# Performance work log

Hardware: AMD Instinct MI355X
Metric: run time of the kernel (lower is better)

The kernel has to match this reference:

```python
import jax, jax.numpy as jnp
import numpy as np

N, E, F0, H = 100000, 3200000, 256, 128
TEMP = 2.0
ALPHA = 0.2  # leaky relu slope
EPS_BN = 1e-5
EPS_LN = 1e-5


def spmm(vals, row, col, X):
    # sparse [N,N] @ dense [N,D] via gather + segment_sum
    return jax.ops.segment_sum(vals[:, None] * X[col], row, num_segments=N)


def batchnorm(h, g, b):
    mu = jnp.mean(h, axis=0, keepdims=True)
    var = jnp.var(h, axis=0, keepdims=True)
    return (h - mu) * jax.lax.rsqrt(var + EPS_BN) * g + b


def layernorm(h, g, b):
    mu = jnp.mean(h, axis=-1, keepdims=True)
    var = jnp.var(h, axis=-1, keepdims=True)
    return (h - mu) * jax.lax.rsqrt(var + EPS_LN) * g + b


def setup_inputs() -> dict:
    key = jax.random.key(0)
    ks = jax.random.split(key, 32)
    x = jax.random.normal(ks[0], (N, F0), dtype=jnp.float32)
    edge_row = jax.random.randint(ks[1], (E,), 0, N)
    edge_col = jax.random.randint(ks[2], (E,), 0, N)
    adj_vals = jax.random.uniform(ks[3], (E,), dtype=jnp.float32) / 32.0  # ~normalized adj
    sf = lambda k, sh: jax.random.normal(k, sh, dtype=jnp.float32) * 0.05
    in_dim = 3 * F0 + 1
    return {
        "x": x, "edge_row": edge_row, "edge_col": edge_col, "adj_vals": adj_vals,
        # LowPassExtractor (GCN)
        "W_gc1": sf(ks[4], (F0, 2 * H)), "b_gc1": jnp.zeros((2 * H,), jnp.float32),
        "bn1_g": jnp.ones((2 * H,), jnp.float32), "bn1_b": jnp.zeros((2 * H,), jnp.float32),
        "W_gc2": sf(ks[5], (2 * H, H)), "b_gc2": jnp.zeros((H,), jnp.float32),
        "bn2_g": jnp.ones((H,), jnp.float32), "bn2_b": jnp.zeros((H,), jnp.float32),
        # Gating
        "Wg1": sf(ks[6], (in_dim, H)), "bg1": jnp.zeros((H,), jnp.float32),
        "ln_g": jnp.ones((H,), jnp.float32), "ln_b": jnp.zeros((H,), jnp.float32),
        "Wg2": sf(ks[7], (H, 2)), "bg2": jnp.zeros((2,), jnp.float32),
        # HighPassExpert
        "Wxp": sf(ks[8], (F0, H)), "bxp": jnp.zeros((H,), jnp.float32),
        "res_scale": jnp.asarray(1.0, jnp.float32),
        "rn_g": jnp.ones((H,), jnp.float32), "rn_b": jnp.zeros((H,), jnp.float32),
        "Wq": sf(ks[9], (H, H)), "Wk": sf(ks[10], (H, H)), "Wv": sf(ks[11], (H, H)),
    }


def reference(x, edge_row, edge_col, adj_vals,
              W_gc1, b_gc1, bn1_g, bn1_b, W_gc2, b_gc2, bn2_g, bn2_b,
              Wg1, bg1, ln_g, ln_b, Wg2, bg2,
              Wxp, bxp, res_scale, rn_g, rn_b, Wq, Wk, Wv):
    # ---- LowPassExtractor: two GCN layers (spmm(adj, xW)+b) with batchnorm+relu
    h1 = jax.nn.relu(batchnorm(spmm(adj_vals, edge_row, edge_col, x @ W_gc1) + b_gc1, bn1_g, bn1_b))
    low = jax.nn.relu(batchnorm(spmm(adj_vals, edge_row, edge_col, h1 @ W_gc2) + b_gc2, bn2_g, bn2_b))

    # ---- Gating: neighborhood stats via spmm
    AX = spmm(adj_vals, edge_row, edge_col, x)
    deg = jax.ops.segment_sum(adj_vals, edge_row, num_segments=N)[:, None]
    x_mean = AX / (deg + 1e-8)
    AX2 = spmm(adj_vals, edge_row, edge_col, x * x)
    var = AX2 / (deg + 1e-8) - x_mean * x_mean
    x_std = jnp.sqrt(jnp.clip(var, 0.0))
    x_cat = jnp.concatenate([x, AX - x, x_std, deg], axis=1)  # [N, 3*F0+1]
    hg = jax.nn.relu(layernorm(x_cat @ Wg1 + bg1, ln_g, ln_b))
    gate = jax.nn.softmax((hg @ Wg2 + bg2) / TEMP, axis=1)  # [N, 2]

    # ---- HighPassExpert: GAT-style sparse attention on normalized residual
    residual = layernorm(res_scale * (x @ Wxp + bxp - low), rn_g, rn_b)
    Q, K, V = residual @ Wq, residual @ Wk, residual @ Wv
    scores = jnp.sum(Q[edge_row] * K[edge_col], axis=1) / jnp.sqrt(jnp.float32(H))
    exp_s = jnp.exp(jnp.where(scores > 0, scores, ALPHA * scores))
    denom = jax.ops.segment_sum(exp_s, edge_row, num_segments=N)
    attn = exp_s / (denom[edge_row] + 1e-16)
    high = jax.ops.segment_sum(attn[:, None] * V[edge_col], edge_row, num_segments=N)

    output = gate[:, 0:1] * low + gate[:, 1:2] * high
    return output, gate, low, high
```

## Files before the change

### kernel.cpp

```cpp
#include <hip/hip_runtime.h>

#define F0 256
#define HD 128
#define NP 100352

typedef unsigned short u16;
typedef __attribute__((ext_vector_type(8))) short short8;
typedef __attribute__((ext_vector_type(4))) float f32x4;

__device__ inline float bf2f(u16 u) {
    union { unsigned int i; float f; } v; v.i = ((unsigned int)u) << 16; return v.f;
}
__device__ inline u16 f2bf(float f) {
    union { float f; unsigned int i; } v; v.f = f;
    unsigned int r = v.i + 0x7FFF + ((v.i >> 16) & 1);
    return (u16)(r >> 16);
}

__device__ inline float rsum16(float v) {
    v += __shfl_xor(v, 1); v += __shfl_xor(v, 2);
    v += __shfl_xor(v, 4); v += __shfl_xor(v, 8);
    return v;
}

#define GLOAD16(gp, lp) __builtin_amdgcn_global_load_lds( \
    (const __attribute__((address_space(1))) void*)(gp), \
    (__attribute__((address_space(3))) void*)(lp), 16, 0, 0)

__global__ void k_hist_rank(const int* __restrict__ row, int* __restrict__ counts,
                            int* __restrict__ rank, int E) {
    int e = blockIdx.x * blockDim.x + threadIdx.x;
    if (e < E) rank[e] = atomicAdd(&counts[row[e]], 1);
}

__global__ void k_scan_blk(const int* __restrict__ counts, int* __restrict__ scan_out,
                           int* __restrict__ partials, int n) {
    __shared__ int wsum[16];
    int t = threadIdx.x;
    int i = blockIdx.x * 1024 + t;
    int v = (i < n) ? counts[i] : 0;
    int lane = t & 63, w = t >> 6;
    #pragma unroll
    for (int off = 1; off < 64; off <<= 1) { int u = __shfl_up(v, off); if (lane >= off) v += u; }
    if (lane == 63) wsum[w] = v;
    __syncthreads();
    if (t < 16) {
        int s = wsum[t];
        #pragma unroll
        for (int off = 1; off < 16; off <<= 1) { int u = __shfl_up(s, off); if (t >= off) s += u; }
        wsum[t] = s;
    }
    __syncthreads();
    int add = (w > 0) ? wsum[w - 1] : 0;
    if (i < n) scan_out[i] = v + add;
    if (t == 1023) partials[blockIdx.x] = wsum[15];
}

__global__ void k_scan_part(int* partials, int nb) {
    __shared__ int ws2[2];
    int t = threadIdx.x;
    int v = (t < nb) ? partials[t] : 0;
    int lane = t & 63, w = t >> 6;
    #pragma unroll
    for (int off = 1; off < 64; off <<= 1) { int u = __shfl_up(v, off); if (lane >= off) v += u; }
    if (lane == 63) ws2[w] = v;
    __syncthreads();
    if (w == 1) v += ws2[0];
    if (t < nb) partials[t] = v;
}

__global__ void k_scan_add(int* __restrict__ row_ptr, const int* __restrict__ partials, int n) {
    int b = blockIdx.x;
    int i = b * 1024 + threadIdx.x;
    if (b == 0 && threadIdx.x == 0) row_ptr[0] = 0;
    int add = (b > 0) ? partials[b - 1] : 0;
    if (i < n) row_ptr[1 + i] += add;
}

__global__ void k_scatter_direct(const int* __restrict__ row, const int* __restrict__ ecol,
                                 const float* __restrict__ avals, const int* __restrict__ rank,
                                 const int* __restrict__ row_ptr, int2* __restrict__ cv, int E) {
    int e = blockIdx.x * blockDim.x + threadIdx.x;
    if (e >= E) return;
    int r = row[e];
    int c = __builtin_nontemporal_load(ecol + e);
    float v = __builtin_nontemporal_load(avals + e);
    int rk = __builtin_nontemporal_load(rank + e);
    int pos = row_ptr[r] + rk;
    cv[pos] = make_int2(c, __float_as_int(v));
}

__global__ void k_cast_x(const float* __restrict__ x, u16* __restrict__ xb, int total4) {
    int i = blockIdx.x * blockDim.x + threadIdx.x;
    if (i >= total4) return;
    float4 v = ((const float4*)x)[i];
    ((ushort4*)xb)[i] = make_ushort4(f2bf(v.x), f2bf(v.y), f2bf(v.z), f2bf(v.w));
}

__global__ void k_prep_w(const float* __restrict__ W_gc1, const float* __restrict__ W_gc2,
                         const float* __restrict__ Wg1, const float* __restrict__ Wxp,
                         const float* __restrict__ Wq, const float* __restrict__ Wk,
                         const float* __restrict__ Wv,
                         u16* Wgc1t, u16* Wgc2t, u16* Wdt, u16* W1t, u16* W2t,
                         u16* Wxpt, u16* Wqt, u16* Wkt, u16* Wvt) {
    int z = blockIdx.z;
    int idx = blockIdx.x * 256 + threadIdx.x;
    if (z == 0) { if (idx < 65536) { int n = idx >> 8, k = idx & 255; Wgc1t[idx] = f2bf(W_gc1[k * 256 + n]); } }
    else if (z == 1) { if (idx < 32768) { int n = idx >> 8, k = idx & 255; Wgc2t[idx] = f2bf(W_gc2[k * 128 + n]); } }
    else if (z == 2) { if (idx < 32768) { int n = idx >> 8, k = idx & 255; Wdt[idx] = f2bf(Wg1[k * 128 + n] - Wg1[(k + 256) * 128 + n]); } }
    else if (z == 3) { if (idx < 32768) { int n = idx >> 8, k = idx & 255; W1t[idx] = f2bf(Wg1[(k + 256) * 128 + n]); } }
    else if (z == 4) { if (idx < 32768) { int n = idx >> 8, k = idx & 255; W2t[idx] = f2bf(Wg1[(k + 512) * 128 + n]); } }
    else if (z == 5) { if (idx < 32768) { int n = idx >> 8, k = idx & 255; Wxpt[idx] = f2bf(Wxp[k * 128 + n]); } }
    else if (z == 6) { if (idx < 16384) { int n = idx >> 7, k = idx & 127; Wqt[idx] = f2bf(Wq[k * 128 + n]); } }
    else if (z == 7) { if (idx < 16384) { int n = idx >> 7, k = idx & 127; Wkt[idx] = f2bf(Wk[k * 128 + n]); } }
    else if (z == 8) { if (idx < 16384) { int n = idx >> 7, k = idx & 127; Wvt[idx] = f2bf(Wv[k * 128 + n]); } }
}

__global__ void k_spmm_x2(const u16* __restrict__ Xb, const int* __restrict__ row_ptr,
                          const int2* __restrict__ cv,
                          u16* __restrict__ AXb, u16* __restrict__ XSTDb,
                          float* __restrict__ deg, int N) {
    int wid = blockIdx.x * 4 + (threadIdx.x >> 6);
    if (wid >= N) return;
    int lane = threadIdx.x & 63;
    float a0 = 0, a1 = 0, a2 = 0, a3 = 0;
    float q0 = 0, q1 = 0, q2 = 0, q3 = 0, d = 0;
    int s = row_ptr[wid], e = row_ptr[wid + 1];
    int j = s;
    for (; j + 7 < e; j += 8) {
        int2 cc[8]; ushort4 xb[8];
        #pragma unroll
        for (int t = 0; t < 8; ++t) cc[t] = cv[j + t];
        #pragma unroll
        for (int t = 0; t < 8; ++t) xb[t] = *(const ushort4*)(Xb + (size_t)cc[t].x * F0 + lane * 4);
        #pragma unroll
        for (int t = 0; t < 8; ++t) {
            float x0 = bf2f(xb[t].x), x1 = bf2f(xb[t].y), x2 = bf2f(xb[t].z), x3 = bf2f(xb[t].w);
            float vv = __int_as_float(cc[t].y);
            a0 += vv * x0; a1 += vv * x1; a2 += vv * x2; a3 += vv * x3;
            q0 += vv * x0 * x0; q1 += vv * x1 * x1; q2 += vv * x2 * x2; q3 += vv * x3 * x3;
            d += vv;
        }
    }
    for (; j < e; ++j) {
        int2 cc = cv[j];
        float v0 = __int_as_float(cc.y);
        ushort4 xb0 = *(const ushort4*)(Xb + (size_t)cc.x * F0 + lane * 4);
        float x0 = bf2f(xb0.x), x1 = bf2f(xb0.y), x2 = bf2f(xb0.z), x3 = bf2f(xb0.w);
        a0 += v0 * x0; a1 += v0 * x1; a2 += v0 * x2; a3 += v0 * x3;
        q0 += v0 * x0 * x0; q1 += v0 * x1 * x1; q2 += v0 * x2 * x2; q3 += v0 * x3 * x3;
        d += v0;
    }
    float inv = 1.0f / (d + 1e-8f);
    float m0 = a0 * inv, m1 = a1 * inv, m2 = a2 * inv, m3 = a3 * inv;
    float s0 = sqrtf(fmaxf(q0 * inv - m0 * m0, 0.f));
    float s1 = sqrtf(fmaxf(q1 * inv - m1 * m1, 0.f));
    float s2 = sqrtf(fmaxf(q2 * inv - m2 * m2, 0.f));
    float s3 = sqrtf(fmaxf(q3 * inv - m3 * m3, 0.f));
    *(ushort4*)(AXb + (size_t)wid * F0 + lane * 4) = make_ushort4(f2bf(a0), f2bf(a1), f2bf(a2), f2bf(a3));
    *(ushort4*)(XSTDb + (size_t)wid * F0 + lane * 4) = make_ushort4(f2bf(s0), f2bf(s1), f2bf(s2), f2bf(s3));
    if (lane == 0) deg[wid] = d;
}

__global__ void k_spmm128(const u16* __restrict__ Xb, const int* __restrict__ row_ptr,
                          const int2* __restrict__ cv, u16* __restrict__ OUT, int N) {
    int wid = blockIdx.x * 4 + (threadIdx.x >> 6);
    if (wid >= N) return;
    int lane = threadIdx.x & 63;
    float a0 = 0, a1 = 0;
    int s = row_ptr[wid], e = row_ptr[wid + 1];
    int j = s;
    for (; j + 7 < e; j += 8) {
        int2 cc[8]; ushort2 xb[8];
        #pragma unroll
        for (int t = 0; t < 8; ++t) cc[t] = cv[j + t];
        #pragma unroll
        for (int t = 0; t < 8; ++t) xb[t] = *(const ushort2*)(Xb + (size_t)cc[t].x * HD + lane * 2);
        #pragma unroll
        for (int t = 0; t < 8; ++t) {
            float vv = __int_as_float(cc[t].y);
            a0 += vv * bf2f(xb[t].x); a1 += vv * bf2f(xb[t].y);
        }
    }
    for (; j < e; ++j) {
        int2 cc = cv[j];
        float v0 = __int_as_float(cc.y);
        ushort2 x0 = *(const ushort2*)(Xb + (size_t)cc.x * HD + lane * 2);
        a0 += v0 * bf2f(x0.x); a1 += v0 * bf2f(x0.y);
    }
    *(ushort2*)(OUT + (size_t)wid * HD + lane * 2) = make_ushort2(f2bf(a0), f2bf(a1));
}

__device__ inline void mm_core(const u16* __restrict__ A, const u16* __restrict__ Bt,
                               int K, int ldA, int ldB, int m0, int n0,
                               u16* As, u16* Bs, f32x4 acc[4][4]) {
    int t = threadIdx.x, w = t >> 6, l = t & 63;
    int wr = (w >> 1) * 64, wc = (w & 1) * 64;
    int aoff = (wr + (l & 15)) * 32 + (l >> 4) * 8;
    int boff = (wc + (l & 15)) * 32 + (l >> 4) * 8;
    for (int k0 = 0; k0 < K; k0 += 32) {
        __syncthreads();
        #pragma unroll
        for (int s = 0; s < 2; ++s) {
            int i = s * 256 + t;
            int row = i >> 2, ch = i & 3;
            GLOAD16(A + (size_t)(m0 + row) * ldA + k0 + ch * 8, As + i * 8);
            GLOAD16(Bt + (size_t)(n0 + row) * ldB + k0 + ch * 8, Bs + i * 8);
        }
        __syncthreads();
        short8 af[4], bfr[4];
        #pragma unroll
        for (int i = 0; i < 4; ++i) af[i] = *(const short8*)(As + aoff + i * 16 * 32);
        #pragma unroll
        for (int j = 0; j < 4; ++j) bfr[j] = *(const short8*)(Bs + boff + j * 16 * 32);
        #pragma unroll
        for (int i = 0; i < 4; ++i)
            #pragma unroll
            for (int j = 0; j < 4; ++j)
                acc[i][j] = __builtin_amdgcn_mfma_f32_16x16x32_bf16(af[i], bfr[j], acc[i][j], 0, 0, 0);
    }
}

__device__ inline void mm_zero(f32x4 acc[4][4]) {
    #pragma unroll
    for (int i = 0; i < 4; ++i)
        #pragma unroll
        for (int j = 0; j < 4; ++j)
            acc[i][j] = (f32x4){0.f, 0.f, 0.f, 0.f};
}

__global__ __launch_bounds__(256) void k_mm_bf(const u16* __restrict__ A, const u16* __restrict__ Bt,
                                               u16* __restrict__ C, int M, int K, int Nc) {
    __shared__ __align__(16) u16 As[128 * 32];
    __shared__ __align__(16) u16 Bs[128 * 32];
    int m0 = blockIdx.x * 128, n0 = blockIdx.y * 128;
    f32x4 acc[4][4]; mm_zero(acc);
    mm_core(A, Bt, K, K, K, m0, n0, As, Bs, acc);
    int t = threadIdx.x, w = t >> 6, l = t & 63;
    int rbase = m0 + (w >> 1) * 64 + (l >> 4) * 4;
    int cbase = n0 + (w & 1) * 64 + (l & 15);
    #pragma unroll
    for (int j = 0; j < 4; ++j)
        #pragma unroll
        for (int i = 0; i < 4; ++i)
            #pragma unroll
            for (int r = 0; r < 4; ++r) {
                int row = rbase + i * 16 + r;
                if (row < M) C[(size_t)row * Nc + cbase + j * 16] = f2bf(acc[i][j][r]);
            }
}

__global__ __launch_bounds__(256) void k_mm_gate(const u16* A0, const u16* A1, const u16* A2,
                                                 const u16* B0, const u16* B1, const u16* B2,
                                                 const float* __restrict__ bg1,
                                                 const float* __restrict__ wlast,
                                                 const float* __restrict__ deg,
                                                 const float* __restrict__ ln_g,
                                                 const float* __restrict__ ln_b,
                                                 const float* __restrict__ Wg2,
                                                 const float* __restrict__ bg2,
                                                 float* __restrict__ gate, int M) {
    __shared__ __align__(16) u16 As[128 * 32];
    __shared__ __align__(16) u16 Bs[128 * 32];
    __shared__ float ps1[2][128], ps2[2][128], pt0[2][128], pt1[2][128];
    int m0 = blockIdx.x * 128;
    f32x4 acc[4][4]; mm_zero(acc);
    mm_core(A0, B0, 256, 256, 256, m0, 0, As, Bs, acc);
    mm_core(A1, B1, 256, 256, 256, m0, 0, As, Bs, acc);
    mm_core(A2, B2, 256, 256, 256, m0, 0, As, Bs, acc);
    int t = threadIdx.x, w = t >> 6, l = t & 63;
    int hcol = w & 1;
    int lr0 = (w >> 1) * 64 + (l >> 4) * 4;
    int cbase = hcol * 64 + (l & 15);
    float wl[4], bg[4], lg[4], lb[4], wa[4], wb_[4];
    #pragma unroll
    for (int j = 0; j < 4; ++j) {
        int col = cbase + j * 16;
        wl[j] = wlast[col]; bg[j] = bg1[col];
        lg[j] = ln_g[col];  lb[j] = ln_b[col];
        wa[j] = Wg2[col * 2 + 0]; wb_[j] = Wg2[col * 2 + 1];
    }
    #pragma unroll
    for (int i = 0; i < 4; ++i)
        #pragma unroll
        for (int r = 0; r < 4; ++r) {
            int row = m0 + lr0 + i * 16 + r;
            float dgv = (row < M) ? deg[row] : 0.f;
            float s1 = 0.f, s2 = 0.f;
            #pragma unroll
            for (int j = 0; j < 4; ++j) {
                float h = acc[i][j][r] + bg[j] + dgv * wl[j];
                acc[i][j][r] = h;
                s1 += h; s2 += h * h;
            }
            s1 = rsum16(s1); s2 = rsum16(s2);
            if ((l & 15) == 0) { ps1[hcol][lr0 + i * 16 + r] = s1; ps2[hcol][lr0 + i * 16 + r] = s2; }
        }
    __syncthreads();
    #pragma unroll
    for (int i = 0; i < 4; ++i)
        #pragma unroll
        for (int r = 0; r < 4; ++r) {
            int lr = lr0 + i * 16 + r;
            float s1 = ps1[0][lr] + ps1[1][lr];
            float s2 = ps2[0][lr] + ps2[1][lr];
            float mu = s1 * (1.f / 128.f);
            float var = s2 * (1.f / 128.f) - mu * mu;
            float is = 1.0f / sqrtf(var + 1e-5f);
            float t0 = 0.f, t1 = 0.f;
            #pragma unroll
            for (int j = 0; j < 4; ++j) {
                float y = fmaxf((acc[i][j][r] - mu) * is * lg[j] + lb[j], 0.f);
                t0 += y * wa[j]; t1 += y * wb_[j];
            }
            t0 = rsum16(t0); t1 = rsum16(t1);
            if ((l & 15) == 0) { pt0[hcol][lr] = t0; pt1[hcol][lr] = t1; }
        }
    __syncthreads();
    if (hcol == 0 && (l & 15) == 0) {
        float b20 = bg2[0], b21 = bg2[1];
        #pragma unroll
        for (int i = 0; i < 4; ++i)
            #pragma unroll
            for (int r = 0; r < 4; ++r) {
                int lr = lr0 + i * 16 + r;
                int row = m0 + lr;
                if (row >= M) continue;
                float t0 = (pt0[0][lr] + pt0[1][lr] + b20) * 0.5f;
                float t1 = (pt1[0][lr] + pt1[1][lr] + b21) * 0.5f;
                float m = fmaxf(t0, t1);
                float e0 = __expf(t0 - m), e1 = __expf(t1 - m);
                float inv = 1.0f / (e0 + e1);
                gate[(size_t)row * 2 + 0] = e0 * inv;
                gate[(size_t)row * 2 + 1] = e1 * inv;
            }
    }
}

__global__ __launch_bounds__(256) void k_mm_xp(const u16* __restrict__ A, const u16* __restrict__ Bt,
                                               const float* __restrict__ bias,
                                               const float* __restrict__ low,
                                               const float* __restrict__ g,
                                               const float* __restrict__ b,
                                               const float* __restrict__ rs_ptr,
                                               u16* __restrict__ resid, int M) {
    __shared__ __align__(16) u16 As[128 * 32];
    __shared__ __align__(16) u16 Bs[128 * 32];
    __shared__ float ps1[2][128], ps2[2][128];
    int m0 = blockIdx.x * 128;
    f32x4 acc[4][4]; mm_zero(acc);
    mm_core(A, Bt, 256, 256, 256, m0, 0, As, Bs, acc);
    int t = threadIdx.x, w = t >> 6, l = t & 63;
    int hcol = w & 1;
    int lr0 = (w >> 1) * 64 + (l >> 4) * 4;
    int cbase = hcol * 64 + (l & 15);
    float rs = rs_ptr[0];
    float bx[4], lg[4], lb[4];
    #pragma unroll
    for (int j = 0; j < 4; ++j) {
        int col = cbase + j * 16;
        bx[j] = bias[col]; lg[j] = g[col]; lb[j] = b[col];
    }
    #pragma unroll
    for (int i = 0; i < 4; ++i)
        #pragma unroll
        for (int r = 0; r < 4; ++r) {
            int row = m0 + lr0 + i * 16 + r;
            float s1 = 0.f, s2 = 0.f;
            #pragma unroll
            for (int j = 0; j < 4; ++j) {
                float lv = (row < M) ? low[(size_t)row * 128 + cbase + j * 16] : 0.f;
                float h = rs * (acc[i][j][r] + bx[j] - lv);
                acc[i][j][r] = h;
                s1 += h; s2 += h * h;
            }
            s1 = rsum16(s1); s2 = rsum16(s2);
            if ((l & 15) == 0) { ps1[hcol][lr0 + i * 16 + r] = s1; ps2[hcol][lr0 + i * 16 + r] = s2; }
        }
    __syncthreads();
    #pragma unroll
    for (int i = 0; i < 4; ++i)
        #pragma unroll
        for (int r = 0; r < 4; ++r) {
            int lr = lr0 + i * 16 + r;
            int row = m0 + lr;
            float s1 = ps1[0][lr] + ps1[1][lr];
            float s2 = ps2[0][lr] + ps2[1][lr];
            float mu = s1 * (1.f / 128.f);
            float var = s2 * (1.f / 128.f) - mu * mu;
            float is = 1.0f / sqrtf(var + 1e-5f);
            if (row < M) {
                #pragma unroll
                for (int j = 0; j < 4; ++j) {
                    float y = (acc[i][j][r] - mu) * is * lg[j] + lb[j];
                    resid[(size_t)row * 128 + cbase + j * 16] = f2bf(y);
                }
            }
        }
}

__global__ __launch_bounds__(256) void k_mm_qkv3(const u16* __restrict__ A,
                                                 const u16* __restrict__ Wqt,
                                                 const u16* __restrict__ Wkt,
                                                 const u16* __restrict__ Wvt,
                                                 u16* __restrict__ Qb, u16* __restrict__ KV, int M) {
    __shared__ __align__(16) u16 As[4][128 * 32];
    __shared__ __align__(16) u16 Bs[128 * 32];
    int m0 = blockIdx.x * 128;
    int t = threadIdx.x, w = t >> 6, l = t & 63;
    #pragma unroll
    for (int c = 0; c < 4; ++c)
        #pragma unroll
        for (int s = 0; s < 2; ++s) {
            int i = s * 256 + t;
            int row = i >> 2, ch = i & 3;
            GLOAD16(A + (size_t)(m0 + row) * 128 + c * 32 + ch * 8, As[c] + i * 8);
        }
    int wr = (w >> 1) * 64, wc = (w & 1) * 64;
    int aoff = (wr + (l & 15)) * 32 + (l >> 4) * 8;
    int boff = (wc + (l & 15)) * 32 + (l >> 4) * 8;
    int rbase = m0 + (w >> 1) * 64 + (l >> 4) * 4;
    int cbase = (w & 1) * 64 + (l & 15);
    #pragma unroll
    for (int z = 0; z < 3; ++z) {
        const u16* Bt = (z == 0) ? Wqt : (z == 1) ? Wkt : Wvt;
        f32x4 acc[4][4]; mm_zero(acc);
        for (int k0 = 0; k0 < 128; k0 += 32) {
            __syncthreads();
            #pragma unroll
            for (int s = 0; s < 2; ++s) {
                int i = s * 256 + t;
                int row = i >> 2, ch = i & 3;
                GLOAD16(Bt + (size_t)row * 128 + k0 + ch * 8, Bs + i * 8);
            }
            __syncthreads();
            const u16* Ac = As[k0 >> 5];
            short8 af[4], bfr[4];
            #pragma unroll
            for (int i = 0; i < 4; ++i) af[i] = *(const short8*)(Ac + aoff + i * 16 * 32);
            #pragma unroll
            for (int j = 0; j < 4; ++j) bfr[j] = *(const short8*)(Bs + boff + j * 16 * 32);
            #pragma unroll
            for (int i = 0; i < 4; ++i)
                #pragma unroll
                for (int j = 0; j < 4; ++j)
                    acc[i][j] = __builtin_amdgcn_mfma_f32_16x16x32_bf16(af[i], bfr[j], acc[i][j], 0, 0, 0);
        }
        if (z == 0) {
            #pragma unroll
            for (int j = 0; j < 4; ++j)
                #pragma unroll
                for (int i = 0; i < 4; ++i)
                    #pragma unroll
                    for (int r = 0; r < 4; ++r) {
                        int row = rbase + i * 16 + r;
                        if (row < M) Qb[(size_t)row * 128 + cbase + j * 16] = f2bf(acc[i][j][r]);
                    }
        } else {
            int coff = (z == 1) ? 0 : 128;
            #pragma unroll
            for (int j = 0; j < 4; ++j)
                #pragma unroll
                for (int i = 0; i < 4; ++i)
                    #pragma unroll
                    for (int r = 0; r < 4; ++r) {
                        int row = rbase + i * 16 + r;
                        if (row < M) KV[(size_t)row * 256 + coff + cbase + j * 16] = f2bf(acc[i][j][r]);
                    }
        }
    }
}

__global__ void k_bn_stats_bf(const u16* __restrict__ H, double* __restrict__ stats, int N, int C) {
    int t = threadIdx.x;
    int rpt = 256 / C;
    int rsub = t / C;
    int col = t - rsub * C;
    double s = 0.0, q = 0.0;
    for (long r = (long)blockIdx.x * rpt + rsub; r < N; r += (long)gridDim.x * rpt) {
        float v = bf2f(H[(size_t)r * C + col]);
        s += v; q += (double)v * v;
    }
    __shared__ double sh_s[256], sh_q[256];
    sh_s[t] = s; sh_q[t] = q;
    __syncthreads();
    if (t < C) {
        for (int k = 1; k < rpt; ++k) { s += sh_s[t + k * C]; q += sh_q[t + k * C]; }
        atomicAdd(&stats[t], s);
        atomicAdd(&stats[C + t], q);
    }
}

__global__ void k_bn_fin(const double* __restrict__ stats, const float* __restrict__ g,
                         const float* __restrict__ b, float* __restrict__ scale,
                         float* __restrict__ shift, int C, double invN) {
    int t = threadIdx.x;
    if (t >= C) return;
    double mean = stats[t] * invN;
    double var = stats[C + t] * invN - mean * mean;
    float sc = (float)((double)g[t] / sqrt(var + 1e-5));
    scale[t] = sc;
    shift[t] = b[t] - (float)mean * sc;
}

__global__ void k_bn_relu_bb(const u16* __restrict__ in, u16* __restrict__ out,
                             const float* __restrict__ scale, const float* __restrict__ shift,
                             int total4, int cmask4) {
    int i = blockIdx.x * blockDim.x + threadIdx.x;
    if (i >= total4) return;
    int c4 = i & cmask4;
    ushort4 v = ((const ushort4*)in)[i];
    float4 sc = ((const float4*)scale)[c4];
    float4 sh = ((const float4*)shift)[c4];
    ((ushort4*)out)[i] = make_ushort4(
        f2bf(fmaxf(bf2f(v.x) * sc.x + sh.x, 0.f)), f2bf(fmaxf(bf2f(v.y) * sc.y + sh.y, 0.f)),
        f2bf(fmaxf(bf2f(v.z) * sc.z + sh.z, 0.f)), f2bf(fmaxf(bf2f(v.w) * sc.w + sh.w, 0.f)));
}

__global__ void k_bn_relu_bf(const u16* __restrict__ in, float* __restrict__ out,
                             const float* __restrict__ scale, const float* __restrict__ shift,
                             int total4, int cmask4) {
    int i = blockIdx.x * blockDim.x + threadIdx.x;
    if (i >= total4) return;
    int c4 = i & cmask4;
    ushort4 v = ((const ushort4*)in)[i];
    float4 sc = ((const float4*)scale)[c4];
    float4 sh = ((const float4*)shift)[c4];
    ((float4*)out)[i] = make_float4(
        fmaxf(bf2f(v.x) * sc.x + sh.x, 0.f), fmaxf(bf2f(v.y) * sc.y + sh.y, 0.f),
        fmaxf(bf2f(v.z) * sc.z + sh.z, 0.f), fmaxf(bf2f(v.w) * sc.w + sh.w, 0.f));
}

__global__ void k_attn_aggr(const u16* __restrict__ Qb, const u16* __restrict__ KV,
                            const int* __restrict__ row_ptr, const int2* __restrict__ cv,
                            const float* __restrict__ gate, const float* __restrict__ low,
                            float* __restrict__ high, float* __restrict__ outp, int N) {
    int wid = blockIdx.x * 4 + (threadIdx.x >> 6);
    if (wid >= N) return;
    int lane = threadIdx.x & 63;
    int sub = lane & 15;
    int g = lane >> 4;
    float qs[8];
    {
        short8 q8 = *(const short8*)(Qb + (size_t)wid * HD + sub * 8);
        #pragma unroll
        for (int k = 0; k < 8; ++k) qs[k] = bf2f((u16)q8[k]);
    }
    float2 qv;
    {
        ushort2 qt = *(const ushort2*)(Qb + (size_t)wid * HD + lane * 2);
        qv.x = bf2f(qt.x); qv.y = bf2f(qt.y);
    }
    float n0 = 0, n1 = 0, den = 0;
    int s = row_ptr[wid], e = row_ptr[wid + 1];
    int j = s;
    for (; j + 7 < e; j += 8) {
        int cg0 = cv[j + g].x;
        int cg1 = cv[j + 4 + g].x;
        short8 ka = *(const short8*)(KV + (size_t)cg0 * 256 + sub * 8);
        short8 kb = *(const short8*)(KV + (size_t)cg1 * 256 + sub * 8);
        float p0 = qs[0] * bf2f((u16)ka[0]) + qs[1] * bf2f((u16)ka[1])
                 + qs[2] * bf2f((u16)ka[2]) + qs[3] * bf2f((u16)ka[3])
                 + qs[4] * bf2f((u16)ka[4]) + qs[5] * bf2f((u16)ka[5])
                 + qs[6] * bf2f((u16)ka[6]) + qs[7] * bf2f((u16)ka[7]);
        float p1 = qs[0] * bf2f((u16)kb[0]) + qs[1] * bf2f((u16)kb[1])
                 + qs[2] * bf2f((u16)kb[2]) + qs[3] * bf2f((u16)kb[3])
                 + qs[4] * bf2f((u16)kb[4]) + qs[5] * bf2f((u16)kb[5])
                 + qs[6] * bf2f((u16)kb[6]) + qs[7] * bf2f((u16)kb[7]);
        p0 += __shfl_xor(p0, 1); p1 += __shfl_xor(p1, 1);
        p0 += __shfl_xor(p0, 2); p1 += __shfl_xor(p1, 2);
        p0 += __shfl_xor(p0, 4); p1 += __shfl_xor(p1, 4);
        p0 += __shfl_xor(p0, 8); p1 += __shfl_xor(p1, 8);
        float sc0 = p0 * 0.08838834764831845f;
        float sc1 = p1 * 0.08838834764831845f;
        float ls0 = sc0 > 0.f ? sc0 : 0.2f * sc0;
        float ls1 = sc1 > 0.f ? sc1 : 0.2f * sc1;
        float ex0 = __expf(ls0);
        float ex1 = __expf(ls1);
        float exb[8]; int cb[8];
        #pragma unroll
        for (int t = 0; t < 4; ++t) {
            exb[t]     = __shfl(ex0, t << 4); cb[t]     = __shfl(cg0, t << 4);
            exb[4 + t] = __shfl(ex1, t << 4); cb[4 + t] = __shfl(cg1, t << 4);
        }
        ushort2 vb[8];
        #pragma unroll
        for (int t = 0; t < 8; ++t) vb[t] = *(const ushort2*)(KV + (size_t)cb[t] * 256 + 128 + lane * 2);
        #pragma unroll
        for (int t = 0; t < 8; ++t) {
            n0 += exb[t] * bf2f(vb[t].x);
            n1 += exb[t] * bf2f(vb[t].y);
            den += exb[t];
        }
    }
    for (; j + 3 < e; j += 4) {
        int cg = cv[j + g].x;
        short8 kk = *(const short8*)(KV + (size_t)cg * 256 + sub * 8);
        float p = qs[0] * bf2f((u16)kk[0]) + qs[1] * bf2f((u16)kk[1])
                + qs[2] * bf2f((u16)kk[2]) + qs[3] * bf2f((u16)kk[3])
                + qs[4] * bf2f((u16)kk[4]) + qs[5] * bf2f((u16)kk[5])
                + qs[6] * bf2f((u16)kk[6]) + qs[7] * bf2f((u16)kk[7]);
        p += __shfl_xor(p, 1); p += __shfl_xor(p, 2);
        p += __shfl_xor(p, 4); p += __shfl_xor(p, 8);
        float sc = p * 0.08838834764831845f;
        float ls = sc > 0.f ? sc : 0.2f * sc;
        float ex = __expf(ls);
        float exb[4]; int cb[4];
        #pragma unroll
        for (int t = 0; t < 4; ++t) { exb[t] = __shfl(ex, t << 4); cb[t] = __shfl(cg, t << 4); }
        ushort2 vb[4];
        #pragma unroll
        for (int t = 0; t < 4; ++t) vb[t] = *(const ushort2*)(KV + (size_t)cb[t] * 256 + 128 + lane * 2);
        #pragma unroll
        for (int t = 0; t < 4; ++t) {
            n0 += exb[t] * bf2f(vb[t].x);
            n1 += exb[t] * bf2f(vb[t].y);
            den += exb[t];
        }
    }
    for (; j < e; ++j) {
        int c0 = cv[j].x;
        ushort2 kb0 = *(const ushort2*)(KV + (size_t)c0 * 256 + lane * 2);
        ushort2 vb0 = *(const ushort2*)(KV + (size_t)c0 * 256 + 128 + lane * 2);
        float sc0 = qv.x * bf2f(kb0.x) + qv.y * bf2f(kb0.y);
        #pragma unroll
        for (int off = 32; off > 0; off >>= 1) sc0 += __shfl_xor(sc0, off);
        float p = sc0 * 0.08838834764831845f;
        float ls = p > 0.f ? p : 0.2f * p;
        float ex = __expf(ls);
        n0 += ex * bf2f(vb0.x); n1 += ex * bf2f(vb0.y); den += ex;
    }
    float inv = 1.0f / (den + 1e-16f);
    float h0 = n0 * inv, h1 = n1 * inv;
    *(float2*)(high + (size_t)wid * HD + lane * 2) = make_float2(h0, h1);
    float g0 = gate[(size_t)wid * 2 + 0], g1 = gate[(size_t)wid * 2 + 1];
    float2 lw = *(const float2*)(low + (size_t)wid * HD + lane * 2);
    *(float2*)(outp + (size_t)wid * HD + lane * 2) = make_float2(g0 * lw.x + g1 * h0, g0 * lw.y + g1 * h1);
}

extern "C" void kernel_launch(void* const* d_in, const int* in_sizes, int n_in,
                              void* d_out, int out_size, void* d_ws, size_t ws_size,
                              hipStream_t stream) {
    const float* x      = (const float*)d_in[0];
    const int*   erow   = (const int*)d_in[1];
    const int*   ecol   = (const int*)d_in[2];
    const float* avals  = (const float*)d_in[3];
    const float* W_gc1  = (const float*)d_in[4];
    const float* bn1_g  = (const float*)d_in[6];
    const float* bn1_b  = (const float*)d_in[7];
    const float* W_gc2  = (const float*)d_in[8];
    const float* bn2_g  = (const float*)d_in[10];
    const float* bn2_b  = (const float*)d_in[11];
    const float* Wg1    = (const float*)d_in[12];
    const float* bg1    = (const float*)d_in[13];
    const float* ln_g   = (const float*)d_in[14];
    const float* ln_b   = (const float*)d_in[15];
    const float* Wg2    = (const float*)d_in[16];
    const float* bg2    = (const float*)d_in[17];
    const float* Wxp    = (const float*)d_in[18];
    const float* bxp    = (const float*)d_in[19];
    const float* rscale = (const float*)d_in[20];
    const float* rn_g   = (const float*)d_in[21];
    const float* rn_b   = (const float*)d_in[22];
    const float* Wq     = (const float*)d_in[23];
    const float* Wk     = (const float*)d_in[24];
    const float* Wv     = (const float*)d_in[25];

    const int N = in_sizes[0] / F0;
    const int E = in_sizes[1];

    char* base = (char*)d_ws;
    size_t off = 0;
    auto carve = [&](size_t bytes) -> char* {
        char* p = base + off;
        off += (bytes + 255) & ~(size_t)255;
        return p;
    };
    double* stats  = (double*)carve(4096);
    float* scaleb  = (float*)carve(1024);
    float* shiftb  = (float*)carve(1024);
    int*   partials= (int*)carve(2048);
    u16* Wgc1t = (u16*)carve(65536 * 2);
    u16* Wgc2t = (u16*)carve(32768 * 2);
    u16* Wdt   = (u16*)carve(32768 * 2);
    u16* W1t   = (u16*)carve(32768 * 2);
    u16* W2t   = (u16*)carve(32768 * 2);
    u16* Wxpt  = (u16*)carve(32768 * 2);
    u16* Wqt   = (u16*)carve(16384 * 2);
    u16* Wkt   = (u16*)carve(16384 * 2);
    u16* Wvt   = (u16*)carve(16384 * 2);
    int*   row_ptr = (int*)carve((size_t)(N + 1) * 4);
    int*   cursor  = (int*)carve((size_t)N * 4);
    float* deg     = (float*)carve((size_t)N * 4);
    int2*  cv      = (int2*)carve((size_t)E * 8);
    u16*   x_bf    = (u16*)carve((size_t)NP * F0 * 2);
    u16*   kvb     = (u16*)carve((size_t)NP * 256 * 2);
    u16*   AX_bf   = (u16*)carve((size_t)NP * F0 * 2);
    u16*   XSTD_bf = (u16*)carve((size_t)NP * F0 * 2);
    u16*   h1_bf   = (u16*)carve((size_t)NP * F0 * 2);
    u16*   S2_bf   = (u16*)carve((size_t)NP * HD * 2);
    u16*   G2_bf   = (u16*)carve((size_t)NP * HD * 2);
    float* M3      = (float*)carve((size_t)NP * HD * 4);
    (void)ws_size; (void)n_in; (void)out_size;

    u16*   S1_bf = h1_bf;
    u16*   resid_bf = h1_bf;
    int*   rank  = (int*)M3;
    u16*   Qb    = (u16*)M3;

    float* out_o    = (float*)d_out;
    float* out_gate = out_o + (size_t)N * HD;
    float* out_low  = out_gate + (size_t)N * 2;
    float* out_high = out_low + (size_t)N * HD;

    const int eb  = (E + 255) / 256;
    const int wb  = (N + 3) / 4;
    const int NB1 = (N + 1023) / 1024;
    const int gx  = (N + 127) / 128;
    const dim3 blk(256);

    hipMemsetAsync(cursor, 0, (size_t)N * 4, stream);
    k_hist_rank<<<eb, blk, 0, stream>>>(erow, cursor, rank, E);
    k_scan_blk<<<NB1, 1024, 0, stream>>>(cursor, row_ptr + 1, partials, N);
    k_scan_part<<<1, 128, 0, stream>>>(partials, NB1);
    k_scan_add<<<NB1, 1024, 0, stream>>>(row_ptr, partials, N);
    k_scatter_direct<<<eb, blk, 0, stream>>>(erow, ecol, avals, rank, row_ptr, cv, E);

    k_cast_x<<<(N * 64 + 255) / 256, blk, 0, stream>>>(x, x_bf, N * 64);
    k_prep_w<<<dim3(256, 1, 9), blk, 0, stream>>>(W_gc1, W_gc2, Wg1, Wxp, Wq, Wk, Wv,
                                                  Wgc1t, Wgc2t, Wdt, W1t, W2t, Wxpt, Wqt, Wkt, Wvt);

    k_spmm_x2<<<wb, blk, 0, stream>>>(x_bf, row_ptr, cv, AX_bf, XSTD_bf, deg, N);

    k_mm_bf<<<dim3(gx, 2), blk, 0, stream>>>(AX_bf, Wgc1t, S1_bf, N, 256, 256);
    hipMemsetAsync(stats, 0, 4096, stream);
    k_bn_stats_bf<<<1024, blk, 0, stream>>>(S1_bf, stats, N, 256);
    k_bn_fin<<<1, blk, 0, stream>>>(stats, bn1_g, bn1_b, scaleb, shiftb, 256, 1.0 / N);
    k_bn_relu_bb<<<(N * 64 + 255) / 256, blk, 0, stream>>>(S1_bf, h1_bf, scaleb, shiftb, N * 64, 63);
    k_mm_bf<<<dim3(gx, 1), blk, 0, stream>>>(h1_bf, Wgc2t, G2_bf, N, 256, 128);
    k_spmm128<<<wb, blk, 0, stream>>>(G2_bf, row_ptr, cv, S2_bf, N);
    hipMemsetAsync(stats, 0, 2048, stream);
    k_bn_stats_bf<<<1024, blk, 0, stream>>>(S2_bf, stats, N, 128);
    k_bn_fin<<<1, blk, 0, stream>>>(stats, bn2_g, bn2_b, scaleb, shiftb, 128, 1.0 / N);
    k_bn_relu_bf<<<(N * 32 + 255) / 256, blk, 0, stream>>>(S2_bf, out_low, scaleb, shiftb, N * 32, 31);

    k_mm_gate<<<dim3(gx, 1), blk, 0, stream>>>(x_bf, AX_bf, XSTD_bf, Wdt, W1t, W2t,
                                               bg1, Wg1 + (size_t)768 * 128, deg,
                                               ln_g, ln_b, Wg2, bg2, out_gate, N);

    k_mm_xp<<<dim3(gx, 1), blk, 0, stream>>>(x_bf, Wxpt, bxp, out_low, rn_g, rn_b, rscale,
                                             resid_bf, N);
    k_mm_qkv3<<<dim3(gx, 1), blk, 0, stream>>>(resid_bf, Wqt, Wkt, Wvt, Qb, kvb, N);
    k_attn_aggr<<<wb, blk, 0, stream>>>(Qb, kvb, row_ptr, cv, out_gate, out_low, out_high, out_o, N);
}
```

Before: 1.530 ms.

## Fuse BN1 stats into GC1 matmul, BN+ReLU into GC2 load, split QKV grid

The first GCN matmul now accumulates per-column sums and sums of squares in its epilogue and adds them to the global stats with double atomics. This removes the separate batch-norm stats pass over S1. The second matmul applies the BN scale/shift and ReLU while loading its A operand, so the standalone bn_relu kernel and the h1 buffer round trip are gone. The QKV kernel is split across a z grid dimension of 3 instead of looping over the three weights in one block, trading A-tile reuse for more parallel blocks. Risks are atomic contention on the stats, and register-staged A loads in GC2 losing the async global-to-LDS path.

```diff
diff --git a/kernel.cpp b/kernel.cpp
--- a/kernel.cpp
+++ b/kernel.cpp
@@ -229,16 +229,20 @@
             acc[i][j] = (f32x4){0.f, 0.f, 0.f, 0.f};
 }
 
-__global__ __launch_bounds__(256) void k_mm_bf(const u16* __restrict__ A, const u16* __restrict__ Bt,
-                                               u16* __restrict__ C, int M, int K, int Nc) {
+__global__ __launch_bounds__(256) void k_mm_gc1(const u16* __restrict__ A, const u16* __restrict__ Bt,
+                                                u16* __restrict__ C, double* __restrict__ stats, int M) {
     __shared__ __align__(16) u16 As[128 * 32];
     __shared__ __align__(16) u16 Bs[128 * 32];
+    __shared__ float cs1[2][128], cs2[2][128];
     int m0 = blockIdx.x * 128, n0 = blockIdx.y * 128;
     f32x4 acc[4][4]; mm_zero(acc);
-    mm_core(A, Bt, K, K, K, m0, n0, As, Bs, acc);
+    mm_core(A, Bt, 256, 256, 256, m0, n0, As, Bs, acc);
     int t = threadIdx.x, w = t >> 6, l = t & 63;
     int rbase = m0 + (w >> 1) * 64 + (l >> 4) * 4;
     int cbase = n0 + (w & 1) * 64 + (l & 15);
+    float sj1[4], sj2[4];
+    #pragma unroll
+    for (int j = 0; j < 4; ++j) { sj1[j] = 0.f; sj2[j] = 0.f; }
     #pragma unroll
     for (int j = 0; j < 4; ++j)
         #pragma unroll
@@ -246,7 +250,101 @@
             #pragma unroll
             for (int r = 0; r < 4; ++r) {
                 int row = rbase + i * 16 + r;
-                if (row < M) C[(size_t)row * Nc + cbase + j * 16] = f2bf(acc[i][j][r]);
+                if (row < M) {
+                    float h = acc[i][j][r];
+                    C[(size_t)row * 256 + cbase + j * 16] = f2bf(h);
+                    sj1[j] += h; sj2[j] += h * h;
+                }
+            }
+    #pragma unroll
+    for (int j = 0; j < 4; ++j) {
+        sj1[j] += __shfl_xor(sj1[j], 16); sj1[j] += __shfl_xor(sj1[j], 32);
+        sj2[j] += __shfl_xor(sj2[j], 16); sj2[j] += __shfl_xor(sj2[j], 32);
+    }
+    if (l < 16) {
+        #pragma unroll
+        for (int j = 0; j < 4; ++j) {
+            int col = (w & 1) * 64 + l + j * 16;
+            cs1[w >> 1][col] = sj1[j];
+            cs2[w >> 1][col] = sj2[j];
+        }
+    }
+    __syncthreads();
+    if (t < 128) {
+        double s = (double)cs1[0][t] + (double)cs1[1][t];
+        atomicAdd(&stats[n0 + t], s);
+    } else {
+        int c = t - 128;
+        double q = (double)cs2[0][c] + (double)cs2[1][c];
+        atomicAdd(&stats[256 + n0 + c], q);
+    }
+}
+
+__global__ __launch_bounds__(256) void k_mm_gc2(const u16* __restrict__ A, const u16* __restrict__ Bt,
+                                                const float* __restrict__ scale,
+                                                const float* __restrict__ shift,
+                                                u16* __restrict__ C, int M) {
+    __shared__ __align__(16) u16 As[128 * 32];
+    __shared__ __align__(16) u16 Bs[128 * 32];
+    int m0 = blockIdx.x * 128;
+    int t = threadIdx.x, w = t >> 6, l = t & 63;
+    int wr = (w >> 1) * 64, wc = (w & 1) * 64;
+    int aoff = (wr + (l & 15)) * 32 + (l >> 4) * 8;
+    int boff = (wc + (l & 15)) * 32 + (l >> 4) * 8;
+    f32x4 acc[4][4]; mm_zero(acc);
+    for (int k0 = 0; k0 < 256; k0 += 32) {
+        short8 av[2];
+        #pragma unroll
+        for (int s = 0; s < 2; ++s) {
+            int i = s * 256 + t;
+            int row = i >> 2, ch = i & 3;
+            int col = k0 + ch * 8;
+            short8 v = *(const short8*)(A + (size_t)(m0 + row) * 256 + col);
+            float4 sa = *(const float4*)(scale + col);
+            float4 sb = *(const float4*)(scale + col + 4);
+            float4 ha = *(const float4*)(shift + col);
+            float4 hb = *(const float4*)(shift + col + 4);
+            short8 o;
+            o[0] = (short)f2bf(fmaxf(bf2f((u16)v[0]) * sa.x + ha.x, 0.f));
+            o[1] = (short)f2bf(fmaxf(bf2f((u16)v[1]) * sa.y + ha.y, 0.f));
+            o[2] = (short)f2bf(fmaxf(bf2f((u16)v[2]) * sa.z + ha.z, 0.f));
+            o[3] = (short)f2bf(fmaxf(bf2f((u16)v[3]) * sa.w + ha.w, 0.f));
+            o[4] = (short)f2bf(fmaxf(bf2f((u16)v[4]) * sb.x + hb.x, 0.f));
+            o[5] = (short)f2bf(fmaxf(bf2f((u16)v[5]) * sb.y + hb.y, 0.f));
+            o[6] = (short)f2bf(fmaxf(bf2f((u16)v[6]) * sb.z + hb.z, 0.f));
+            o[7] = (short)f2bf(fmaxf(bf2f((u16)v[7]) * sb.w + hb.w, 0.f));
+            av[s] = o;
+        }
+        __syncthreads();
+        #pragma unroll
+        for (int s = 0; s < 2; ++s) {
+            int i = s * 256 + t;
+            *(short8*)(As + i * 8) = av[s];
+            int row = i >> 2, ch = i & 3;
+            GLOAD16(Bt + (size_t)row * 256 + k0 + ch * 8, Bs + i * 8);
+        }
+        __syncthreads();
+        short8 af[4], bfr[4];
+        #pragma unroll
+        for (int i = 0; i < 4; ++i) af[i] = *(const short8*)(As + aoff + i * 16 * 32);
+        #pragma unroll
+        for (int j = 0; j < 4; ++j) bfr[j] = *(const short8*)(Bs + boff + j * 16 * 32);
+        #pragma unroll
+        for (int i = 0; i < 4; ++i)
+            #pragma unroll
+            for (int j = 0; j < 4; ++j)
+                acc[i][j] = __builtin_amdgcn_mfma_f32_16x16x32_bf16(af[i], bfr[j], acc[i][j], 0, 0, 0);
+    }
+    int rbase = m0 + (w >> 1) * 64 + (l >> 4) * 4;
+    int cbase = (w & 1) * 64 + (l & 15);
+    #pragma unroll
+    for (int j = 0; j < 4; ++j)
+        #pragma unroll
+        for (int i = 0; i < 4; ++i)
+            #pragma unroll
+            for (int r = 0; r < 4; ++r) {
+                int row = rbase + i * 16 + r;
+                if (row < M) C[(size_t)row * 128 + cbase + j * 16] = f2bf(acc[i][j][r]);
             }
 }
 
@@ -399,75 +497,40 @@
         }
 }
 
-__global__ __launch_bounds__(256) void k_mm_qkv3(const u16* __restrict__ A,
-                                                 const u16* __restrict__ Wqt,
-                                                 const u16* __restrict__ Wkt,
-                                                 const u16* __restrict__ Wvt,
-                                                 u16* __restrict__ Qb, u16* __restrict__ KV, int M) {
-    __shared__ __align__(16) u16 As[4][128 * 32];
+__global__ __launch_bounds__(256) void k_mm_qkv(const u16* __restrict__ A,
+                                                const u16* Wqt, const u16* Wkt, const u16* Wvt,
+                                                u16* Qb, u16* KV, int M) {
+    __shared__ __align__(16) u16 As[128 * 32];
     __shared__ __align__(16) u16 Bs[128 * 32];
+    int z = blockIdx.z;
+    const u16* Bt = (z == 0) ? Wqt : (z == 1) ? Wkt : Wvt;
     int m0 = blockIdx.x * 128;
+    f32x4 acc[4][4]; mm_zero(acc);
+    mm_core(A, Bt, 128, 128, 128, m0, 0, As, Bs, acc);
     int t = threadIdx.x, w = t >> 6, l = t & 63;
-    #pragma unroll
-    for (int c = 0; c < 4; ++c)
-        #pragma unroll
-        for (int s = 0; s < 2; ++s) {
-            int i = s * 256 + t;
-            int row = i >> 2, ch = i & 3;
-            GLOAD16(A + (size_t)(m0 + row) * 128 + c * 32 + ch * 8, As[c] + i * 8);
-        }
-    int wr = (w >> 1) * 64, wc = (w & 1) * 64;
-    int aoff = (wr + (l & 15)) * 32 + (l >> 4) * 8;
-    int boff = (wc + (l & 15)) * 32 + (l >> 4) * 8;
     int rbase = m0 + (w >> 1) * 64 + (l >> 4) * 4;
     int cbase = (w & 1) * 64 + (l & 15);
-    #pragma unroll
-    for (int z = 0; z < 3; ++z) {
-        const u16* Bt = (z == 0) ? Wqt : (z == 1) ? Wkt : Wvt;
-        f32x4 acc[4][4]; mm_zero(acc);
-        for (int k0 = 0; k0 < 128; k0 += 32) {
-            __syncthreads();
-            #pragma unroll
-            for (int s = 0; s < 2; ++s) {
-                int i = s * 256 + t;
-                int row = i >> 2, ch = i & 3;
-                GLOAD16(Bt + (size_t)row * 128 + k0 + ch * 8, Bs + i * 8);
-            }
-            __syncthreads();
-            const u16* Ac = As[k0 >> 5];
-            short8 af[4], bfr[4];
-            #pragma unroll
-            for (int i = 0; i < 4; ++i) af[i] = *(const short8*)(Ac + aoff + i * 16 * 32);
-            #pragma unroll
-            for (int j = 0; j < 4; ++j) bfr[j] = *(const short8*)(Bs + boff + j * 16 * 32);
+    if (z == 0) {
+        #pragma unroll
+        for (int j = 0; j < 4; ++j)
             #pragma unroll
             for (int i = 0; i < 4; ++i)
                 #pragma unroll
-                for (int j = 0; j < 4; ++j)
-                    acc[i][j] = __builtin_amdgcn_mfma_f32_16x16x32_bf16(af[i], bfr[j], acc[i][j], 0, 0, 0);
-        }
-        if (z == 0) {
-            #pragma unroll
-            for (int j = 0; j < 4; ++j)
+                for (int r = 0; r < 4; ++r) {
+                    int row = rbase + i * 16 + r;
+                    if (row < M) Qb[(size_t)row * 128 + cbase + j * 16] = f2bf(acc[i][j][r]);
+                }
+    } else {
+        int coff = (z == 1) ? 0 : 128;
+        #pragma unroll
+        for (int j = 0; j < 4; ++j)
+            #pragma unroll
+            for (int i = 0; i < 4; ++i)
                 #pragma unroll
-                for (int i = 0; i < 4; ++i)
-                    #pragma unroll
-                    for (int r = 0; r < 4; ++r) {
-                        int row = rbase + i * 16 + r;
-                        if (row < M) Qb[(size_t)row * 128 + cbase + j * 16] = f2bf(acc[i][j][r]);
-                    }
-        } else {
-            int coff = (z == 1) ? 0 : 128;
-            #pragma unroll
-            for (int j = 0; j < 4; ++j)
-                #pragma unroll
-                for (int i = 0; i < 4; ++i)
-                    #pragma unroll
-                    for (int r = 0; r < 4; ++r) {
-                        int row = rbase + i * 16 + r;
-                        if (row < M) KV[(size_t)row * 256 + coff + cbase + j * 16] = f2bf(acc[i][j][r]);
-                    }
-        }
+                for (int r = 0; r < 4; ++r) {
+                    int row = rbase + i * 16 + r;
+                    if (row < M) KV[(size_t)row * 256 + coff + cbase + j * 16] = f2bf(acc[i][j][r]);
+                }
     }
 }
 
@@ -501,20 +564,6 @@
     float sc = (float)((double)g[t] / sqrt(var + 1e-5));
     scale[t] = sc;
     shift[t] = b[t] - (float)mean * sc;
-}
-
-__global__ void k_bn_relu_bb(const u16* __restrict__ in, u16* __restrict__ out,
-                             const float* __restrict__ scale, const float* __restrict__ shift,
-                             int total4, int cmask4) {
-    int i = blockIdx.x * blockDim.x + threadIdx.x;
-    if (i >= total4) return;
-    int c4 = i & cmask4;
-    ushort4 v = ((const ushort4*)in)[i];
-    float4 sc = ((const float4*)scale)[c4];
-    float4 sh = ((const float4*)shift)[c4];
-    ((ushort4*)out)[i] = make_ushort4(
-        f2bf(fmaxf(bf2f(v.x) * sc.x + sh.x, 0.f)), f2bf(fmaxf(bf2f(v.y) * sc.y + sh.y, 0.f)),
-        f2bf(fmaxf(bf2f(v.z) * sc.z + sh.z, 0.f)), f2bf(fmaxf(bf2f(v.w) * sc.w + sh.w, 0.f)));
 }
 
 __global__ void k_bn_relu_bf(const u16* __restrict__ in, float* __restrict__ out,
@@ -732,12 +781,10 @@
 
     k_spmm_x2<<<wb, blk, 0, stream>>>(x_bf, row_ptr, cv, AX_bf, XSTD_bf, deg, N);
 
-    k_mm_bf<<<dim3(gx, 2), blk, 0, stream>>>(AX_bf, Wgc1t, S1_bf, N, 256, 256);
     hipMemsetAsync(stats, 0, 4096, stream);
-    k_bn_stats_bf<<<1024, blk, 0, stream>>>(S1_bf, stats, N, 256);
+    k_mm_gc1<<<dim3(gx, 2), blk, 0, stream>>>(AX_bf, Wgc1t, S1_bf, stats, N);
     k_bn_fin<<<1, blk, 0, stream>>>(stats, bn1_g, bn1_b, scaleb, shiftb, 256, 1.0 / N);
-    k_bn_relu_bb<<<(N * 64 + 255) / 256, blk, 0, stream>>>(S1_bf, h1_bf, scaleb, shiftb, N * 64, 63);
-    k_mm_bf<<<dim3(gx, 1), blk, 0, stream>>>(h1_bf, Wgc2t, G2_bf, N, 256, 128);
+    k_mm_gc2<<<dim3(gx, 1), blk, 0, stream>>>(S1_bf, Wgc2t, scaleb, shiftb, G2_bf, N);
     k_spmm128<<<wb, blk, 0, stream>>>(G2_bf, row_ptr, cv, S2_bf, N);
     hipMemsetAsync(stats, 0, 2048, stream);
     k_bn_stats_bf<<<1024, blk, 0, stream>>>(S2_bf, stats, N, 128);
@@ -750,6 +797,6 @@
 
     k_mm_xp<<<dim3(gx, 1), blk, 0, stream>>>(x_bf, Wxpt, bxp, out_low, rn_g, rn_b, rscale,
                                              resid_bf, N);
-    k_mm_qkv3<<<dim3(gx, 1), blk, 0, stream>>>(resid_bf, Wqt, Wkt, Wvt, Qb, kvb, N);
+    k_mm_qkv<<<dim3(gx, 1, 3), blk, 0, stream>>>(resid_bf, Wqt, Wkt, Wvt, Qb, kvb, N);
     k_attn_aggr<<<wb, blk, 0, stream>>>(Qb, kvb, row_ptr, cv, out_gate, out_low, out_high, out_o, N);
 }
```

New measurement: 1.362 ms. -10.9%, faster.
